# Performance work log

Measured on AMD Instinct MI355X. Metric: run time of the kernel, lower is better.

## Reference

```python
import jax, jax.numpy as jnp
import numpy as np


def setup_inputs() -> dict:
    key = jax.random.key(0)
    k0, k1, k2 = jax.random.split(key, 3)
    B, C, H, W = 16, 256, 64, 64
    features = jax.random.normal(k0, (B, C, H, W), dtype=jnp.float32)
    # tiny 3->16->1 MLP params (PyTorch Linear layout transposed to (in, out))
    W1 = jax.random.normal(k1, (3, 16), dtype=jnp.float32) * (1.0 / np.sqrt(3.0))
    b1 = jnp.zeros((16,), dtype=jnp.float32)
    W2 = jax.random.normal(k2, (16, 1), dtype=jnp.float32) * (1.0 / np.sqrt(16.0))
    b2 = jnp.zeros((1,), dtype=jnp.float32)
    return {"features": features, "W1": W1, "b1": b1, "W2": W2, "b2": b2}


def reference(features, W1, b1, W2, b2):
    # features: (B, C, H, W). Per-pixel channel stats over C, then 3->16->1 MLP.
    C = features.shape[1]
    # magnitude = ||f||_2 / sqrt(C) = sqrt(mean(f^2))
    sq_mean = jnp.mean(features * features, axis=1)          # (B, H, W)
    mag = jnp.sqrt(sq_mean)
    # torch.var / torch.std use unbiased (ddof=1) estimators
    var = jnp.var(features, axis=1, ddof=1)                  # (B, H, W)
    std = jnp.sqrt(var)
    mag = jnp.clip(mag, 0.0, 1.0)
    var = jnp.clip(var, 0.0, 1.0)
    grad = jnp.clip(std, 0.0, 1.0)
    x = jnp.stack([mag, var, grad], axis=-1)                 # (B, H, W, 3)
    h = jax.nn.relu(jnp.einsum('bhwi,io->bhwo', x, W1) + b1) # (B, H, W, 16)
    out = jax.nn.sigmoid(jnp.einsum('bhwi,io->bhwo', h, W2) + b2)  # (B, H, W, 1)
    return out[..., 0]                                       # (B, H, W)
```

## Files before the change

kernel.cpp:

```cpp
#include <hip/hip_runtime.h>


#define C_DIM 256
#define HW4   1024

__global__ __launch_bounds__(512, 8) void fis_importance_kernel(
    const float* __restrict__ features,
    const float* __restrict__ W1,
    const float* __restrict__ b1,
    const float* __restrict__ W2,
    const float* __restrict__ b2,
    float* __restrict__ out)
{
    const int row = blockIdx.x;
    const int tid = threadIdx.x;
    const int w4  = tid & 15;
    const int cg  = tid >> 4;

    const int b = row >> 6;
    const int h = row & 63;

    const float4* fptr = reinterpret_cast<const float4*>(features)
        + ((size_t)(b * C_DIM + cg * 8) * 64 + h) * 16 + w4;

    float4 s = make_float4(0.f, 0.f, 0.f, 0.f);
    float4 q = make_float4(0.f, 0.f, 0.f, 0.f);

#pragma unroll
    for (int batch = 0; batch < 2; ++batch) {
        float4 v0 = fptr[(size_t)(batch * 4 + 0) * HW4];
        float4 v1 = fptr[(size_t)(batch * 4 + 1) * HW4];
        float4 v2 = fptr[(size_t)(batch * 4 + 2) * HW4];
        float4 v3 = fptr[(size_t)(batch * 4 + 3) * HW4];
        s.x += v0.x + v1.x + v2.x + v3.x;
        s.y += v0.y + v1.y + v2.y + v3.y;
        s.z += v0.z + v1.z + v2.z + v3.z;
        s.w += v0.w + v1.w + v2.w + v3.w;
        q.x += v0.x*v0.x + v1.x*v1.x + v2.x*v2.x + v3.x*v3.x;
        q.y += v0.y*v0.y + v1.y*v1.y + v2.y*v2.y + v3.y*v3.y;
        q.z += v0.z*v0.z + v1.z*v1.z + v2.z*v2.z + v3.z*v3.z;
        q.w += v0.w*v0.w + v1.w*v1.w + v2.w*v2.w + v3.w*v3.w;
    }

    __shared__ float4 s_sum[32][16];
    __shared__ float4 s_sq [32][16];
    s_sum[cg][w4] = s;
    s_sq [cg][w4] = q;
    __syncthreads();

    if (tid < 64) {
        const int w   = tid;
        const int ww4 = w >> 2;
        const int j   = w & 3;

        float sum = 0.f, sq = 0.f;
#pragma unroll
        for (int g = 0; g < 32; ++g) {
            sum += reinterpret_cast<const float*>(&s_sum[g][ww4])[j];
            sq  += reinterpret_cast<const float*>(&s_sq [g][ww4])[j];
        }

        const float inv_c  = 1.0f / 256.0f;
        const float inv_c1 = 1.0f / 255.0f;

        float mag = sqrtf(sq * inv_c);
        float var = (sq - sum * sum * inv_c) * inv_c1;
        var = fmaxf(var, 0.f);
        float stdv = sqrtf(var);

        mag = fminf(fmaxf(mag, 0.f), 1.f);
        float varc = fminf(var,  1.f);
        float grad = fminf(stdv, 1.f);

        float o = b2[0];
#pragma unroll
        for (int k = 0; k < 16; ++k) {
            float hk = b1[k] + mag * W1[k] + varc * W1[16 + k] + grad * W1[32 + k];
            hk = fmaxf(hk, 0.f);
            o += hk * W2[k];
        }
        out[row * 64 + w] = 1.f / (1.f + __expf(-o));
    }
}

extern "C" void kernel_launch(void* const* d_in, const int* in_sizes, int n_in,
                              void* d_out, int out_size, void* d_ws, size_t ws_size,
                              hipStream_t stream) {
    const float* features = (const float*)d_in[0];
    const float* W1 = (const float*)d_in[1];
    const float* b1 = (const float*)d_in[2];
    const float* W2 = (const float*)d_in[3];
    const float* b2 = (const float*)d_in[4];
    float* out = (float*)d_out;

    fis_importance_kernel<<<1024, 512, 0, stream>>>(features, W1, b1, W2, b2, out);
}
```

Baseline: 96.12 us.

## Process four rows per block with 1024 threads and 16 channels per thread

Reorganizes the grid so each block covers four image rows (256 pixels) with 1024 threads, each thread accumulating 16 channels instead of 8. Each wavefront now reads 1KB contiguous spans rather than 256B, and per-thread memory-level parallelism doubles. The trade-off is a quarter as many blocks and larger blocks, which changes occupancy and tail behaviour. Only a quarter of the threads do the final reduction and MLP.

```diff
diff --git a/kernel.cpp b/kernel.cpp
--- a/kernel.cpp
+++ b/kernel.cpp
@@ -2,9 +2,9 @@
 
 
 #define C_DIM 256
-#define HW4   1024
+#define PLANE4 1024
 
-__global__ __launch_bounds__(512, 8) void fis_importance_kernel(
+__global__ __launch_bounds__(1024, 4) void fis_importance_kernel(
     const float* __restrict__ features,
     const float* __restrict__ W1,
     const float* __restrict__ b1,
@@ -12,26 +12,25 @@
     const float* __restrict__ b2,
     float* __restrict__ out)
 {
-    const int row = blockIdx.x;
+    const int blk = blockIdx.x;
+    const int b   = blk >> 4;
+    const int h0  = (blk & 15) << 2;
     const int tid = threadIdx.x;
-    const int w4  = tid & 15;
-    const int cg  = tid >> 4;
-
-    const int b = row >> 6;
-    const int h = row & 63;
+    const int p4  = tid & 63;
+    const int cg  = tid >> 6;
 
     const float4* fptr = reinterpret_cast<const float4*>(features)
-        + ((size_t)(b * C_DIM + cg * 8) * 64 + h) * 16 + w4;
+        + ((size_t)(b * C_DIM + cg * 16) * 64 + h0) * 16 + p4;
 
     float4 s = make_float4(0.f, 0.f, 0.f, 0.f);
     float4 q = make_float4(0.f, 0.f, 0.f, 0.f);
 
 #pragma unroll
-    for (int batch = 0; batch < 2; ++batch) {
-        float4 v0 = fptr[(size_t)(batch * 4 + 0) * HW4];
-        float4 v1 = fptr[(size_t)(batch * 4 + 1) * HW4];
-        float4 v2 = fptr[(size_t)(batch * 4 + 2) * HW4];
-        float4 v3 = fptr[(size_t)(batch * 4 + 3) * HW4];
+    for (int batch = 0; batch < 4; ++batch) {
+        float4 v0 = fptr[(size_t)(batch * 4 + 0) * PLANE4];
+        float4 v1 = fptr[(size_t)(batch * 4 + 1) * PLANE4];
+        float4 v2 = fptr[(size_t)(batch * 4 + 2) * PLANE4];
+        float4 v3 = fptr[(size_t)(batch * 4 + 3) * PLANE4];
         s.x += v0.x + v1.x + v2.x + v3.x;
         s.y += v0.y + v1.y + v2.y + v3.y;
         s.z += v0.z + v1.z + v2.z + v3.z;
@@ -42,22 +41,20 @@
         q.w += v0.w*v0.w + v1.w*v1.w + v2.w*v2.w + v3.w*v3.w;
     }
 
-    __shared__ float4 s_sum[32][16];
-    __shared__ float4 s_sq [32][16];
-    s_sum[cg][w4] = s;
-    s_sq [cg][w4] = q;
+    __shared__ float4 s_sum[16][64];
+    __shared__ float4 s_sq [16][64];
+    s_sum[cg][p4] = s;
+    s_sq [cg][p4] = q;
     __syncthreads();
 
-    if (tid < 64) {
-        const int w   = tid;
-        const int ww4 = w >> 2;
-        const int j   = w & 3;
+    if (tid < 256) {
+        const int p = tid;
 
         float sum = 0.f, sq = 0.f;
 #pragma unroll
-        for (int g = 0; g < 32; ++g) {
-            sum += reinterpret_cast<const float*>(&s_sum[g][ww4])[j];
-            sq  += reinterpret_cast<const float*>(&s_sq [g][ww4])[j];
+        for (int g = 0; g < 16; ++g) {
+            sum += reinterpret_cast<const float*>(&s_sum[g][p >> 2])[p & 3];
+            sq  += reinterpret_cast<const float*>(&s_sq [g][p >> 2])[p & 3];
         }
 
         const float inv_c  = 1.0f / 256.0f;
@@ -79,7 +76,7 @@
             hk = fmaxf(hk, 0.f);
             o += hk * W2[k];
         }
-        out[row * 64 + w] = 1.f / (1.f + __expf(-o));
+        out[((b * 64 + h0) * 64) + p] = 1.f / (1.f + __expf(-o));
     }
 }
 
@@ -93,5 +90,5 @@
     const float* b2 = (const float*)d_in[4];
     float* out = (float*)d_out;
 
-    fis_importance_kernel<<<1024, 512, 0, stream>>>(features, W1, b1, W2, b2, out);
+    fis_importance_kernel<<<256, 1024, 0, stream>>>(features, W1, b1, W2, b2, out);
 }
```

Measured after the change: 100.1 us. 4.1% more time.
